# Kernel optimization log

Measured on AMD Instinct MI355X. Metric: run time of the kernel, lower is better.

## Reference

```python
import jax, jax.numpy as jnp
import numpy as np

N_NODES = 50000
N_EDGES = 800000
HEADS = 4
NEG_SLOPE = 0.2  # DGL GATConv default and act1 slope


def _gat_layer(x, src, dst, W, al, ar, b, n_nodes, heads, dh):
    # x: [N, Fin] -> proj: [N, H, Dh]
    proj = (x @ W).reshape(n_nodes, heads, dh)
    el = jnp.einsum('nhd,hd->nh', proj, al)  # [N, H]
    er = jnp.einsum('nhd,hd->nh', proj, ar)  # [N, H]
    e = jax.nn.leaky_relu(el[src] + er[dst], NEG_SLOPE)  # [E, H]
    # segment softmax over incoming edges of each dst node
    m = jax.ops.segment_max(e, dst, num_segments=n_nodes)
    m = jnp.where(jnp.isfinite(m), m, jnp.zeros_like(m))
    ex = jnp.exp(e - m[dst])
    s = jax.ops.segment_sum(ex, dst, num_segments=n_nodes)
    alpha = ex / (s[dst] + 1e-9)  # [E, H]
    msg = proj[src] * alpha[:, :, None]  # [E, H, Dh]
    out = jax.ops.segment_sum(msg, dst, num_segments=n_nodes)  # [N, H, Dh]
    return out.reshape(n_nodes, heads * dh) + b


def setup_inputs() -> dict:
    key = jax.random.key(0)
    ks = jax.random.split(key, 10)
    d = {
        'init_emb': jax.random.normal(ks[0], (N_NODES, 300), jnp.float32) * 0.1,
        'W1': jax.random.normal(ks[1], (300, 400), jnp.float32) * (1.0 / np.sqrt(300)),
        'al1': jax.random.normal(ks[2], (HEADS, 100), jnp.float32) * 0.1,
        'ar1': jax.random.normal(ks[3], (HEADS, 100), jnp.float32) * 0.1,
        'b1': jnp.zeros((400,), jnp.float32),
        'W2': jax.random.normal(ks[4], (400, 512), jnp.float32) * (1.0 / np.sqrt(400)),
        'al2': jax.random.normal(ks[5], (HEADS, 128), jnp.float32) * 0.1,
        'ar2': jax.random.normal(ks[6], (HEADS, 128), jnp.float32) * 0.1,
        'b2': jnp.zeros((512,), jnp.float32),
        'src': jax.random.randint(ks[7], (N_EDGES,), 0, N_NODES, jnp.int32),
        'dst': jax.random.randint(ks[8], (N_EDGES,), 0, N_NODES, jnp.int32),
    }
    return d


def reference(init_emb, W1, al1, ar1, b1, W2, al2, ar2, b2, src, dst):
    x = _gat_layer(init_emb, src, dst, W1, al1, ar1, b1, N_NODES, HEADS, 100)  # [N, 400]
    x = jax.nn.leaky_relu(x, NEG_SLOPE)  # act1
    x = _gat_layer(x, src, dst, W2, al2, ar2, b2, N_NODES, HEADS, 128)  # [N, 512]
    return x
```

## Files before the change

### kernel.cpp

```cpp
#include <hip/hip_runtime.h>
#include <math.h>
#include <stdint.h>

#define NN 50000
#define NE 800000
#define HEADS 4

typedef __attribute__((ext_vector_type(8))) short bf16x8;
typedef __attribute__((ext_vector_type(4))) float f32x4;

__device__ __forceinline__ uint32_t bf16rne(float x) {
  uint32_t b = __float_as_uint(x);
  return (b + 0x7FFFu + ((b >> 16) & 1u)) >> 16;
}
__device__ __forceinline__ float bflo(uint32_t v) {
  return __uint_as_float(v << 16);
}
__device__ __forceinline__ float bfhi(uint32_t v) {
  return __uint_as_float(v & 0xFFFF0000u);
}

__global__ void hist_kernel(const int* __restrict__ dst, int* __restrict__ counts, int n) {
  int i = blockIdx.x * blockDim.x + threadIdx.x;
  if (i < n) atomicAdd(&counts[dst[i]], 1);
}

__global__ void scan_kernel(const int* __restrict__ counts, int* __restrict__ row_ptr, int n) {
  __shared__ int wsum[16];
  const int lane = threadIdx.x & 63;
  const int w = threadIdx.x >> 6;
  int carry = 0;
  for (int start = 0; start < n; start += 1024) {
    int i = start + (int)threadIdx.x;
    int v = (i < n) ? counts[i] : 0;
    int x = v;
#pragma unroll
    for (int off = 1; off < 64; off <<= 1) {
      int t = __shfl_up(x, off);
      if (lane >= off) x += t;
    }
    if (lane == 63) wsum[w] = x;
    __syncthreads();
    if (w == 0 && lane < 16) {
      int s = wsum[lane];
#pragma unroll
      for (int off = 1; off < 16; off <<= 1) {
        int t = __shfl_up(s, off);
        if (lane >= off) s += t;
      }
      wsum[lane] = s;
    }
    __syncthreads();
    int woff = (w > 0) ? wsum[w - 1] : 0;
    int incl = x + woff;
    if (i < n) row_ptr[i] = carry + incl - v;
    carry += wsum[15];
    __syncthreads();
  }
  if (threadIdx.x == 0) row_ptr[n] = carry;
}

__global__ void scatter_kernel(const int* __restrict__ dst, const int* __restrict__ src,
                               const int* __restrict__ row_ptr, int* __restrict__ cursor,
                               int* __restrict__ srcs, int n) {
  int i = blockIdx.x * blockDim.x + threadIdx.x;
  if (i < n) {
    int d = dst[i];
    int pos = atomicAdd(&cursor[d], 1);
    srcs[row_ptr[d] + pos] = src[i];
  }
}

__global__ void build_bt3(const float* __restrict__ B, unsigned short* __restrict__ BT3,
                          int K, int N, int K3p) {
  int kp = blockIdx.x * blockDim.x + threadIdx.x;
  int n = blockIdx.y;
  if (kp >= K3p) return;
  unsigned short out = 0;
  if (n < N && kp < 3 * K) {
    int k = kp / 3;
    int r = kp - 3 * k;
    float v = B[(size_t)k * N + n];
    uint32_t hi = bf16rne(v);
    if (r == 1) {
      float back = __uint_as_float(hi << 16);
      out = (unsigned short)bf16rne(v - back);
    } else {
      out = (unsigned short)hi;
    }
  }
  BT3[(size_t)n * K3p + kp] = out;
}

__global__ __launch_bounds__(256, 2) void gemm_split3(
    const float* __restrict__ A, const unsigned short* __restrict__ BT3,
    unsigned short* __restrict__ Ch, int M, int K, int K3p, int Nst) {
  __shared__ unsigned short As[128 * 96];
  __shared__ unsigned short Bs[128 * 96];
  const int tid = threadIdx.x;
  const int w = tid >> 6, lane = tid & 63;
  const int wr = w >> 1, wc = w & 1;
  const int ln = lane & 15, quad = lane >> 4;
  const int m0 = blockIdx.y * 128, n0 = blockIdx.x * 128;
  const int ar = tid >> 1, ah = tid & 1;
  const long arow = (long)min(m0 + ar, M - 1) * K;

  f32x4 acc[4][4];
#pragma unroll
  for (int mi = 0; mi < 4; ++mi)
#pragma unroll
    for (int ni = 0; ni < 4; ++ni) acc[mi][ni] = (f32x4){0.f, 0.f, 0.f, 0.f};

  const int ksteps = (K + 31) / 32;
  for (int s = 0; s < ksteps; ++s) {
    const int k0 = s * 32;
    const int kp0 = s * 96;
#pragma unroll
    for (int j = 0; j < 6; ++j) {
      int g = (w * 6 + j) * 64 + lane;
      unsigned row = ((unsigned)g * 5462u) >> 16;
      unsigned col = (unsigned)g - row * 12u;
      const unsigned short* gp = BT3 + (size_t)(n0 + row) * K3p + kp0 + col * 8;
      void* lp = (void*)((char*)Bs + (size_t)(w * 6 + j) * 1024);
      __builtin_amdgcn_global_load_lds(
          (const __attribute__((address_space(1))) void*)gp,
          (__attribute__((address_space(3))) void*)lp, 16, 0, 0);
    }
    {
      float f[16];
      const int kb = k0 + ah * 16;
#pragma unroll
      for (int q = 0; q < 4; ++q) {
        int gk = kb + q * 4;
        if (gk + 3 < K) {
          *(float4*)&f[q * 4] = *(const float4*)&A[arow + gk];
        } else {
#pragma unroll
          for (int t = 0; t < 4; ++t) f[q * 4 + t] = (gk + t < K) ? A[arow + gk + t] : 0.f;
        }
      }
      unsigned short tr[48];
#pragma unroll
      for (int j = 0; j < 16; ++j) {
        uint32_t hi = bf16rne(f[j]);
        float back = __uint_as_float(hi << 16);
        uint32_t lo = bf16rne(f[j] - back);
        tr[3 * j + 0] = (unsigned short)hi;
        tr[3 * j + 1] = (unsigned short)hi;
        tr[3 * j + 2] = (unsigned short)lo;
      }
      uint32_t u[24];
#pragma unroll
      for (int i = 0; i < 24; ++i)
        u[i] = (uint32_t)tr[2 * i] | ((uint32_t)tr[2 * i + 1] << 16);
      uint4* dst = (uint4*)((char*)As + ar * 192 + ah * 96);
#pragma unroll
      for (int t = 0; t < 6; ++t) dst[t] = *(uint4*)&u[t * 4];
    }
    __syncthreads();
#pragma unroll
    for (int sub = 0; sub < 3; ++sub) {
      bf16x8 af[4], bfr[4];
#pragma unroll
      for (int mi = 0; mi < 4; ++mi)
        af[mi] = *(const bf16x8*)&As[(wr * 64 + mi * 16 + ln) * 96 + sub * 32 + quad * 8];
#pragma unroll
      for (int ni = 0; ni < 4; ++ni)
        bfr[ni] = *(const bf16x8*)&Bs[(wc * 64 + ni * 16 + ln) * 96 + sub * 32 + quad * 8];
#pragma unroll
      for (int mi = 0; mi < 4; ++mi)
#pragma unroll
        for (int ni = 0; ni < 4; ++ni)
          acc[mi][ni] =
              __builtin_amdgcn_mfma_f32_16x16x32_bf16(af[mi], bfr[ni], acc[mi][ni], 0, 0, 0);
    }
    __syncthreads();
  }
#pragma unroll
  for (int mi = 0; mi < 4; ++mi) {
#pragma unroll
    for (int r = 0; r < 4; ++r) {
      int gm = m0 + wr * 64 + mi * 16 + quad * 4 + r;
      if (gm < M) {
        unsigned short* crow = Ch + (size_t)gm * Nst;
#pragma unroll
        for (int ni = 0; ni < 4; ++ni) {
          int gn = n0 + wc * 64 + ni * 16 + ln;
          if (gn < Nst) crow[gn] = (unsigned short)bf16rne(acc[mi][ni][r]);
        }
      }
    }
  }
}

template <int DH>
__global__ void el_er_kernel(const unsigned short* __restrict__ projh,
                             const float* __restrict__ al, const float* __restrict__ ar,
                             float* __restrict__ el, float* __restrict__ er) {
  int t = blockIdx.x * blockDim.x + threadIdx.x;
  if (t >= NN * HEADS) return;
  int h = t & (HEADS - 1);
  const unsigned short* pr = projh + (size_t)t * DH;
  const float* alh = al + h * DH;
  const float* arh = ar + h * DH;
  float sl = 0.f, sr = 0.f;
#pragma unroll 4
  for (int d = 0; d < DH; d += 4) {
    uint2 pv = *(const uint2*)&pr[d];
    float p0 = bflo(pv.x), p1 = bfhi(pv.x), p2 = bflo(pv.y), p3 = bfhi(pv.y);
    float4 av = *(const float4*)&alh[d];
    float4 rv = *(const float4*)&arh[d];
    sl += p0 * av.x + p1 * av.y + p2 * av.z + p3 * av.w;
    sr += p0 * rv.x + p1 * rv.y + p2 * rv.z + p3 * rv.w;
  }
  el[t] = sl;
  er[t] = sr;
}

template <int DH, bool ACT>
__global__ __launch_bounds__(256) void aggregate_kernel(
    const unsigned short* __restrict__ projh, const float* __restrict__ el,
    const float* __restrict__ er, const float* __restrict__ bias,
    const int* __restrict__ row_ptr, const int* __restrict__ srcs,
    float* __restrict__ out) {
  constexpr int HALF = DH / 2;
  const int n = blockIdx.x;
  const int h = threadIdx.x >> 6;
  const int lane = threadIdx.x & 63;
  const bool active = lane < HALF;
  const int beg = row_ptr[n], end = row_ptr[n + 1];
  const float er_nh = er[n * HEADS + h];
  const uint32_t* base = (const uint32_t*)projh;
  float l = 0.f, accx = 0.f, accy = 0.f;
  int i = beg;
  for (; i + 3 < end; i += 4) {
    int s0 = srcs[i], s1 = srcs[i + 1], s2 = srcs[i + 2], s3 = srcs[i + 3];
    float e0 = el[s0 * HEADS + h] + er_nh;
    float e1 = el[s1 * HEADS + h] + er_nh;
    float e2 = el[s2 * HEADS + h] + er_nh;
    float e3 = el[s3 * HEADS + h] + er_nh;
    e0 = (e0 > 0.f) ? e0 : 0.2f * e0;
    e1 = (e1 > 0.f) ? e1 : 0.2f * e1;
    e2 = (e2 > 0.f) ? e2 : 0.2f * e2;
    e3 = (e3 > 0.f) ? e3 : 0.2f * e3;
    uint32_t v0 = 0, v1 = 0, v2 = 0, v3 = 0;
    if (active) {
      v0 = base[((size_t)s0 * HEADS + h) * HALF + lane];
      v1 = base[((size_t)s1 * HEADS + h) * HALF + lane];
      v2 = base[((size_t)s2 * HEADS + h) * HALF + lane];
      v3 = base[((size_t)s3 * HEADS + h) * HALF + lane];
    }
    float p0 = __expf(e0), p1 = __expf(e1), p2 = __expf(e2), p3 = __expf(e3);
    l += (p0 + p1) + (p2 + p3);
    accx += p0 * bflo(v0) + p1 * bflo(v1) + p2 * bflo(v2) + p3 * bflo(v3);
    accy += p0 * bfhi(v0) + p1 * bfhi(v1) + p2 * bfhi(v2) + p3 * bfhi(v3);
  }
  for (; i < end; ++i) {
    int s0 = srcs[i];
    float e0 = el[s0 * HEADS + h] + er_nh;
    e0 = (e0 > 0.f) ? e0 : 0.2f * e0;
    uint32_t v0 = 0;
    if (active) v0 = base[((size_t)s0 * HEADS + h) * HALF + lane];
    float p0 = __expf(e0);
    l += p0;
    accx += p0 * bflo(v0);
    accy += p0 * bfhi(v0);
  }
  float inv = 1.f / (l + 1e-9f);
  if (active) {
    float2 bv = *(const float2*)&bias[h * DH + 2 * lane];
    float ox = accx * inv + bv.x;
    float oy = accy * inv + bv.y;
    if (ACT) {
      ox = (ox > 0.f) ? ox : 0.2f * ox;
      oy = (oy > 0.f) ? oy : 0.2f * oy;
    }
    *(float2*)&out[((size_t)n * HEADS + h) * DH + 2 * lane] = make_float2(ox, oy);
  }
}

extern "C" void kernel_launch(void* const* d_in, const int* in_sizes, int n_in,
                              void* d_out, int out_size, void* d_ws, size_t ws_size,
                              hipStream_t stream) {
  const float* init_emb = (const float*)d_in[0];
  const float* W1 = (const float*)d_in[1];
  const float* al1 = (const float*)d_in[2];
  const float* ar1 = (const float*)d_in[3];
  const float* b1 = (const float*)d_in[4];
  const float* W2 = (const float*)d_in[5];
  const float* al2 = (const float*)d_in[6];
  const float* ar2 = (const float*)d_in[7];
  const float* b2 = (const float*)d_in[8];
  const int* src = (const int*)d_in[9];
  const int* dst = (const int*)d_in[10];
  float* out = (float*)d_out;

  char* ws = (char*)d_ws;
  size_t off = 0;
  auto alloc = [&](size_t bytes) {
    void* p = ws + off;
    off += (bytes + 255) & ~((size_t)255);
    return p;
  };
  unsigned short* projh = (unsigned short*)alloc((size_t)NN * 512 * 2);
  float* x1 = (float*)alloc((size_t)NN * 400 * 4);
  float* el = (float*)alloc((size_t)NN * HEADS * 4);
  float* er = (float*)alloc((size_t)NN * HEADS * 4);
  unsigned short* BT3 = (unsigned short*)alloc((size_t)512 * 1248 * 2);
  int* row_ptr = (int*)alloc((size_t)(NN + 1) * 4);
  int* counts = (int*)alloc((size_t)NN * 4);
  int* srcs = (int*)alloc((size_t)NE * 4);

  hipMemsetAsync(counts, 0, (size_t)NN * 4, stream);
  hist_kernel<<<(NE + 255) / 256, 256, 0, stream>>>(dst, counts, NE);
  scan_kernel<<<1, 1024, 0, stream>>>(counts, row_ptr, NN);
  hipMemsetAsync(counts, 0, (size_t)NN * 4, stream);
  scatter_kernel<<<(NE + 255) / 256, 256, 0, stream>>>(dst, src, row_ptr, counts, srcs, NE);

  build_bt3<<<dim3((960 + 255) / 256, 512), 256, 0, stream>>>(W1, BT3, 300, 400, 960);
  gemm_split3<<<dim3(4, (NN + 127) / 128), 256, 0, stream>>>(init_emb, BT3, projh, NN, 300, 960, 400);
  el_er_kernel<100><<<(NN * HEADS + 255) / 256, 256, 0, stream>>>(projh, al1, ar1, el, er);
  aggregate_kernel<100, true><<<NN, 256, 0, stream>>>(projh, el, er, b1, row_ptr, srcs, x1);

  build_bt3<<<dim3((1248 + 255) / 256, 512), 256, 0, stream>>>(W2, BT3, 400, 512, 1248);
  gemm_split3<<<dim3(4, (NN + 127) / 128), 256, 0, stream>>>(x1, BT3, projh, NN, 400, 1248, 512);
  el_er_kernel<128><<<(NN * HEADS + 255) / 256, 256, 0, stream>>>(projh, al2, ar2, el, er);
  aggregate_kernel<128, false><<<NN, 256, 0, stream>>>(projh, el, er, b2, row_ptr, srcs, out);
}
```

Measured before the change: 795.5 us.

## Pad per-head projection rows and aggregate one node per wavefront with 16B gathers

The GEMM epilogue now writes projections in a padded per-head layout (100→104 columns per head for layer 1), so each head row is 16-byte aligned. A new aggregation kernel maps one node to each wavefront instead of one node per 256-thread block. Each lane gathers 8 bf16 values per edge with a uint4 load, and edge weights are computed 16 edges at a time and broadcast with shuffles. This is meant to cut per-block overhead, raise memory-level parallelism and vectorise the gathers. The cost is a padded buffer with a few wasted lanes and more shuffle instructions.

```diff
diff --git a/kernel.cpp b/kernel.cpp
--- a/kernel.cpp
+++ b/kernel.cpp
@@ -94,7 +94,8 @@
 
 __global__ __launch_bounds__(256, 2) void gemm_split3(
     const float* __restrict__ A, const unsigned short* __restrict__ BT3,
-    unsigned short* __restrict__ Ch, int M, int K, int K3p, int Nst) {
+    unsigned short* __restrict__ Ch, int M, int K, int K3p, int NstR, int RSc,
+    int DHR, int DHP, int magic) {
   __shared__ unsigned short As[128 * 96];
   __shared__ unsigned short Bs[128 * 96];
   const int tid = threadIdx.x;
@@ -182,30 +183,35 @@
     for (int r = 0; r < 4; ++r) {
       int gm = m0 + wr * 64 + mi * 16 + quad * 4 + r;
       if (gm < M) {
-        unsigned short* crow = Ch + (size_t)gm * Nst;
+        unsigned short* crow = Ch + (size_t)gm * RSc;
 #pragma unroll
         for (int ni = 0; ni < 4; ++ni) {
           int gn = n0 + wc * 64 + ni * 16 + ln;
-          if (gn < Nst) crow[gn] = (unsigned short)bf16rne(acc[mi][ni][r]);
+          if (gn < NstR) {
+            int h = (gn * magic) >> 12;
+            int col = h * DHP + (gn - h * DHR);
+            crow[col] = (unsigned short)bf16rne(acc[mi][ni][r]);
+          }
         }
       }
     }
   }
 }
 
-template <int DH>
+template <int DHR, int DHP>
 __global__ void el_er_kernel(const unsigned short* __restrict__ projh,
                              const float* __restrict__ al, const float* __restrict__ ar,
                              float* __restrict__ el, float* __restrict__ er) {
   int t = blockIdx.x * blockDim.x + threadIdx.x;
   if (t >= NN * HEADS) return;
   int h = t & (HEADS - 1);
-  const unsigned short* pr = projh + (size_t)t * DH;
-  const float* alh = al + h * DH;
-  const float* arh = ar + h * DH;
+  int n = t >> 2;
+  const unsigned short* pr = projh + (size_t)n * (HEADS * DHP) + (size_t)h * DHP;
+  const float* alh = al + h * DHR;
+  const float* arh = ar + h * DHR;
   float sl = 0.f, sr = 0.f;
 #pragma unroll 4
-  for (int d = 0; d < DH; d += 4) {
+  for (int d = 0; d < DHR; d += 4) {
     uint2 pv = *(const uint2*)&pr[d];
     float p0 = bflo(pv.x), p1 = bfhi(pv.x), p2 = bflo(pv.y), p3 = bfhi(pv.y);
     float4 av = *(const float4*)&alh[d];
@@ -217,65 +223,106 @@
   er[t] = sr;
 }
 
-template <int DH, bool ACT>
-__global__ __launch_bounds__(256) void aggregate_kernel(
+template <int DHP, int DHR, bool ACT>
+__global__ __launch_bounds__(256) void aggregate2(
     const unsigned short* __restrict__ projh, const float* __restrict__ el,
     const float* __restrict__ er, const float* __restrict__ bias,
     const int* __restrict__ row_ptr, const int* __restrict__ srcs,
     float* __restrict__ out) {
-  constexpr int HALF = DH / 2;
-  const int n = blockIdx.x;
-  const int h = threadIdx.x >> 6;
+  constexpr int LPH = DHP / 8;
+  constexpr int RS = HEADS * DHP * 2;
+  const int node = blockIdx.x * 4 + (threadIdx.x >> 6);
+  if (node >= NN) return;
   const int lane = threadIdx.x & 63;
-  const bool active = lane < HALF;
-  const int beg = row_ptr[n], end = row_ptr[n + 1];
-  const float er_nh = er[n * HEADS + h];
-  const uint32_t* base = (const uint32_t*)projh;
-  float l = 0.f, accx = 0.f, accy = 0.f;
+  const int beg = row_ptr[node], end = row_ptr[node + 1];
+  const int e16 = lane >> 2, hp = lane & 3;
+  const float er_p = er[node * 4 + hp];
+  int head;
+  if constexpr (LPH == 16) head = lane >> 4;
+  else head = (lane * 5) >> 6;
+  const int u = lane - head * LPH;
+  const int laneByte = head * (DHP * 2) + u * 16;
+  const bool active = lane < 4 * LPH;
+  const char* pb = (const char*)projh;
+
+  float bv[8];
+  const int d0 = u * 8;
+#pragma unroll
+  for (int j = 0; j < 8; ++j)
+    bv[j] = (active && d0 + j < DHR) ? bias[head * DHR + d0 + j] : 0.f;
+
+  float acc[8];
+#pragma unroll
+  for (int j = 0; j < 8; ++j) acc[j] = 0.f;
+  float lsum = 0.f;
+
   int i = beg;
-  for (; i + 3 < end; i += 4) {
-    int s0 = srcs[i], s1 = srcs[i + 1], s2 = srcs[i + 2], s3 = srcs[i + 3];
-    float e0 = el[s0 * HEADS + h] + er_nh;
-    float e1 = el[s1 * HEADS + h] + er_nh;
-    float e2 = el[s2 * HEADS + h] + er_nh;
-    float e3 = el[s3 * HEADS + h] + er_nh;
-    e0 = (e0 > 0.f) ? e0 : 0.2f * e0;
-    e1 = (e1 > 0.f) ? e1 : 0.2f * e1;
-    e2 = (e2 > 0.f) ? e2 : 0.2f * e2;
-    e3 = (e3 > 0.f) ? e3 : 0.2f * e3;
-    uint32_t v0 = 0, v1 = 0, v2 = 0, v3 = 0;
-    if (active) {
-      v0 = base[((size_t)s0 * HEADS + h) * HALF + lane];
-      v1 = base[((size_t)s1 * HEADS + h) * HALF + lane];
-      v2 = base[((size_t)s2 * HEADS + h) * HALF + lane];
-      v3 = base[((size_t)s3 * HEADS + h) * HALF + lane];
-    }
-    float p0 = __expf(e0), p1 = __expf(e1), p2 = __expf(e2), p3 = __expf(e3);
-    l += (p0 + p1) + (p2 + p3);
-    accx += p0 * bflo(v0) + p1 * bflo(v1) + p2 * bflo(v2) + p3 * bflo(v3);
-    accy += p0 * bfhi(v0) + p1 * bfhi(v1) + p2 * bfhi(v2) + p3 * bfhi(v3);
-  }
-  for (; i < end; ++i) {
-    int s0 = srcs[i];
-    float e0 = el[s0 * HEADS + h] + er_nh;
-    e0 = (e0 > 0.f) ? e0 : 0.2f * e0;
-    uint32_t v0 = 0;
-    if (active) v0 = base[((size_t)s0 * HEADS + h) * HALF + lane];
-    float p0 = __expf(e0);
-    l += p0;
-    accx += p0 * bflo(v0);
-    accy += p0 * bfhi(v0);
-  }
-  float inv = 1.f / (l + 1e-9f);
+  for (; i + 16 <= end; i += 16) {
+    int sE = srcs[i + e16];
+    float ev = el[sE * 4 + hp] + er_p;
+    ev = fmaxf(ev, 0.2f * ev);
+    float pv_ = __expf(ev);
+    int off_ = sE * RS;
+#pragma unroll
+    for (int e = 0; e < 16; ++e) {
+      const int sl = e * 4 + head;
+      const float pv = __shfl(pv_, sl);
+      const int off = __shfl(off_, sl);
+      uint4 q = *(const uint4*)(pb + (uint32_t)(off + laneByte));
+      lsum += pv;
+      acc[0] += pv * bflo(q.x);
+      acc[1] += pv * bfhi(q.x);
+      acc[2] += pv * bflo(q.y);
+      acc[3] += pv * bfhi(q.y);
+      acc[4] += pv * bflo(q.z);
+      acc[5] += pv * bfhi(q.z);
+      acc[6] += pv * bflo(q.w);
+      acc[7] += pv * bfhi(q.w);
+    }
+  }
+  if (i < end) {
+    const int rem = end - i;
+    int sE = 0;
+    float pv_ = 0.f;
+    if (e16 < rem) {
+      sE = srcs[i + e16];
+      float ev = el[sE * 4 + hp] + er_p;
+      ev = fmaxf(ev, 0.2f * ev);
+      pv_ = __expf(ev);
+    }
+    int off_ = sE * RS;
+#pragma unroll
+    for (int e = 0; e < 16; ++e) {
+      if (e < rem) {
+        const int sl = e * 4 + head;
+        const float pv = __shfl(pv_, sl);
+        const int off = __shfl(off_, sl);
+        uint4 q = *(const uint4*)(pb + (uint32_t)(off + laneByte));
+        lsum += pv;
+        acc[0] += pv * bflo(q.x);
+        acc[1] += pv * bfhi(q.x);
+        acc[2] += pv * bflo(q.y);
+        acc[3] += pv * bfhi(q.y);
+        acc[4] += pv * bflo(q.z);
+        acc[5] += pv * bfhi(q.z);
+        acc[6] += pv * bflo(q.w);
+        acc[7] += pv * bfhi(q.w);
+      }
+    }
+  }
+
+  const float inv = 1.f / (lsum + 1e-9f);
   if (active) {
-    float2 bv = *(const float2*)&bias[h * DH + 2 * lane];
-    float ox = accx * inv + bv.x;
-    float oy = accy * inv + bv.y;
-    if (ACT) {
-      ox = (ox > 0.f) ? ox : 0.2f * ox;
-      oy = (oy > 0.f) ? oy : 0.2f * oy;
-    }
-    *(float2*)&out[((size_t)n * HEADS + h) * DH + 2 * lane] = make_float2(ox, oy);
+    float o[8];
+#pragma unroll
+    for (int j = 0; j < 8; ++j) {
+      float v = acc[j] * inv + bv[j];
+      if (ACT) v = (v > 0.f) ? v : 0.2f * v;
+      o[j] = v;
+    }
+    float* orow = out + (size_t)node * (HEADS * DHR) + head * DHR + d0;
+    *(float4*)orow = make_float4(o[0], o[1], o[2], o[3]);
+    if (d0 + 7 < DHR) *(float4*)(orow + 4) = make_float4(o[4], o[5], o[6], o[7]);
   }
 }
 
@@ -318,12 +365,14 @@
   scatter_kernel<<<(NE + 255) / 256, 256, 0, stream>>>(dst, src, row_ptr, counts, srcs, NE);
 
   build_bt3<<<dim3((960 + 255) / 256, 512), 256, 0, stream>>>(W1, BT3, 300, 400, 960);
-  gemm_split3<<<dim3(4, (NN + 127) / 128), 256, 0, stream>>>(init_emb, BT3, projh, NN, 300, 960, 400);
-  el_er_kernel<100><<<(NN * HEADS + 255) / 256, 256, 0, stream>>>(projh, al1, ar1, el, er);
-  aggregate_kernel<100, true><<<NN, 256, 0, stream>>>(projh, el, er, b1, row_ptr, srcs, x1);
+  gemm_split3<<<dim3(4, (NN + 127) / 128), 256, 0, stream>>>(init_emb, BT3, projh, NN, 300, 960,
+                                                             400, 416, 100, 104, 41);
+  el_er_kernel<100, 104><<<(NN * HEADS + 255) / 256, 256, 0, stream>>>(projh, al1, ar1, el, er);
+  aggregate2<104, 100, true><<<(NN + 3) / 4, 256, 0, stream>>>(projh, el, er, b1, row_ptr, srcs, x1);
 
   build_bt3<<<dim3((1248 + 255) / 256, 512), 256, 0, stream>>>(W2, BT3, 400, 512, 1248);
-  gemm_split3<<<dim3(4, (NN + 127) / 128), 256, 0, stream>>>(x1, BT3, projh, NN, 400, 1248, 512);
-  el_er_kernel<128><<<(NN * HEADS + 255) / 256, 256, 0, stream>>>(projh, al2, ar2, el, er);
-  aggregate_kernel<128, false><<<NN, 256, 0, stream>>>(projh, el, er, b2, row_ptr, srcs, out);
-}
+  gemm_split3<<<dim3(4, (NN + 127) / 128), 256, 0, stream>>>(x1, BT3, projh, NN, 400, 1248,
+                                                             512, 512, 128, 128, 32);
+  el_er_kernel<128, 128><<<(NN * HEADS + 255) / 256, 256, 0, stream>>>(projh, al2, ar2, el, er);
+  aggregate2<128, 128, false><<<(NN + 3) / 4, 256, 0, stream>>>(projh, el, er, b2, row_ptr, srcs, out);
+}
```

Result: no change. 803.1 us (+1.0%).
